# Kernel optimization log

Measured on AMD Instinct MI355X. Metric: run time of the kernel, lower is better.

## Reference

```python
import jax, jax.numpy as jnp
import numpy as np


def log_g(x):
    # log of g(x) = where(x>=0, x+0.5, sigmoid(x))
    return jnp.where(x >= 0, jnp.log(jnp.maximum(x, 0) + 0.5), -jax.nn.softplus(-x))


def setup_inputs() -> dict:
    key = jax.random.key(0)
    ks = jax.random.split(key, 6)
    B, S, D, H = 4, 4096, 1024, 1024
    x = jax.random.normal(ks[0], (B, S, D), dtype=jnp.float32)
    h0 = jax.random.normal(ks[1], (B, 1, H), dtype=jnp.float32)
    # Linear params (scaled like trained weights to keep activations tame)
    Wz = jax.random.normal(ks[2], (H, D), dtype=jnp.float32) * 0.02
    bz = jax.random.normal(ks[3], (H,), dtype=jnp.float32) * 0.02
    Wh = jax.random.normal(ks[4], (H, D), dtype=jnp.float32) * 0.02
    bh = jax.random.normal(ks[5], (H,), dtype=jnp.float32) * 0.02
    return {"x": x, "h0": h0, "Wz": Wz, "bz": bz, "Wh": Wh, "bh": bh}


def reference(x, h0, Wz, bz, Wh, bh):
    # x: [B,S,D], h0: [B,1,H]
    k = jnp.einsum('bsd,hd->bsh', x, Wz) + bz            # linear_z(x)
    log_z = -jax.nn.softplus(-k)                          # log sigmoid(k)
    log_coeffs = -jax.nn.softplus(k)                      # log (1 - sigmoid(k))
    log_h0 = log_g(h0)                                    # [B,1,H]
    log_tilde_h = log_g(jnp.einsum('bsd,hd->bsh', x, Wh) + bh)
    log_coeffs = jnp.pad(log_coeffs, ((0, 0), (1, 0), (0, 0)))  # prepend zero coeff
    log_values = jnp.concatenate([log_h0, log_z + log_tilde_h], axis=1)  # [B,S+1,H]
    # parallel scan in log space
    a_star = jnp.cumsum(log_coeffs, axis=1)
    log_h = a_star + jax.lax.cumlogsumexp(log_values - a_star, axis=1)
    h = jnp.exp(log_h)
    out = h[:, 1:]                                        # last seq_len steps
    return (out, out[:, -1:])
```

## Files before the change

kernel.cpp:

```cpp
#include <hip/hip_runtime.h>
#include <stdint.h>

typedef __attribute__((ext_vector_type(4))) float f32x4;
typedef __attribute__((ext_vector_type(8))) short bf16x8;
typedef __attribute__((ext_vector_type(4))) unsigned short u16x4;

constexpr int cB = 4, cS = 4096, cD = 1024, cH = 1024;
constexpr int cM = cB * cS;
constexpr int cK = cD;
constexpr int NCH = 64;
constexpr int CLEN = cS / NCH;

__device__ __forceinline__ unsigned short f2bf(float f) {
  union { float f; uint32_t u; } v; v.f = f;
  uint32_t r = v.u + 0x7FFFu + ((v.u >> 16) & 1u);
  return (unsigned short)(r >> 16);
}
__device__ __forceinline__ float bf2f(unsigned short h) {
  union { float f; uint32_t u; } v; v.u = ((uint32_t)h) << 16;
  return v.f;
}

__global__ void round_kernel(const float* __restrict__ src,
                             unsigned short* __restrict__ hi) {
  int i = (blockIdx.x * blockDim.x + threadIdx.x) * 4;
  f32x4 x = *(const f32x4*)(src + i);
  u16x4 h;
#pragma unroll
  for (int j = 0; j < 4; ++j) h[j] = f2bf(x[j]);
  *(u16x4*)(hi + i) = h;
}

constexpr int BM = 128, BN = 128, BK = 64;

__global__ __launch_bounds__(256, 2) void gemm_kernel(
    const unsigned short* __restrict__ xh,
    const unsigned short* __restrict__ wwh,
    const float* __restrict__ bz, const float* __restrict__ bhv,
    unsigned short* __restrict__ cbuf, unsigned short* __restrict__ gbuf,
    float* __restrict__ Pb, float* __restrict__ Qb)
{
  __shared__ unsigned short Ah[BM * BK], Bz[BN * BK], Bh[BN * BK];
  const int tid  = threadIdx.x;
  const int lane = tid & 63;
  const int wv   = tid >> 6;
  const int wr   = wv >> 1, wc = wv & 1;

  const int bid = blockIdx.x;
  const int xcd = bid & 7;
  const int idx = bid >> 3;
  const int mt  = xcd * 16 + (idx >> 3);
  const int nt  = idx & 7;
  const int m0 = mt * BM, n0 = nt * BN;
  const int fr = lane & 15, fq = lane >> 4;

  f32x4 accz[4][4] = {};
  f32x4 acch[4][4] = {};

  const int srow = tid >> 3;
  const int scol = (((tid & 7) ^ (srow & 7)) << 3);

  const unsigned short* gA = xh  + (size_t)m0 * cK;
  const unsigned short* gZ = wwh + (size_t)n0 * cK;
  const unsigned short* gH = wwh + (size_t)(cH + n0) * cK;

  for (int kt = 0; kt < cK / BK; ++kt) {
    const int k0 = kt * BK;
    __syncthreads();
#pragma unroll
    for (int r = 0; r < 4; ++r) {
      const int row = r * 32 + srow;
      const int ldsoff = r * 4096 + tid * 16;
      const size_t goff = (size_t)row * cK + k0 + scol;
      __builtin_amdgcn_global_load_lds((const __attribute__((address_space(1))) void*)(gA + goff),
        (__attribute__((address_space(3))) void*)((char*)Ah + ldsoff), 16, 0, 0);
      __builtin_amdgcn_global_load_lds((const __attribute__((address_space(1))) void*)(gZ + goff),
        (__attribute__((address_space(3))) void*)((char*)Bz + ldsoff), 16, 0, 0);
      __builtin_amdgcn_global_load_lds((const __attribute__((address_space(1))) void*)(gH + goff),
        (__attribute__((address_space(3))) void*)((char*)Bh + ldsoff), 16, 0, 0);
    }
    __syncthreads();
#pragma unroll
    for (int kk = 0; kk < BK / 32; ++kk) {
      bf16x8 fa[4], fz[4], fh[4];
#pragma unroll
      for (int i = 0; i < 4; ++i) {
        const int ar = wr * 64 + i * 16 + fr;
        const int ca = (kk * 64 + fq * 16) ^ ((ar & 7) << 4);
        fa[i] = *(const bf16x8*)((const char*)Ah + ar * 128 + ca);
        const int br = wc * 64 + i * 16 + fr;
        const int cb = (kk * 64 + fq * 16) ^ ((br & 7) << 4);
        fz[i] = *(const bf16x8*)((const char*)Bz + br * 128 + cb);
        fh[i] = *(const bf16x8*)((const char*)Bh + br * 128 + cb);
      }
#pragma unroll
      for (int i = 0; i < 4; ++i)
#pragma unroll
        for (int j = 0; j < 4; ++j) {
          accz[i][j] = __builtin_amdgcn_mfma_f32_16x16x32_bf16(fa[i], fz[j], accz[i][j], 0, 0, 0);
          acch[i][j] = __builtin_amdgcn_mfma_f32_16x16x32_bf16(fa[i], fh[j], acch[i][j], 0, 0, 0);
        }
    }
  }

  const int b  = mt >> 5;
  const int ch = (mt & 31) * 2 + wr;
#pragma unroll
  for (int j = 0; j < 4; ++j) {
    const int n = n0 + wc * 64 + j * 16 + fr;
    const float bz_n = bz[n];
    const float bh_n = bhv[n];
    float psg[4], qsg[4];
#pragma unroll
    for (int i = 0; i < 4; ++i) {
      float p = 1.0f, q = 0.0f;
#pragma unroll
      for (int rg = 0; rg < 4; ++rg) {
        const int m = m0 + wr * 64 + i * 16 + fq * 4 + rg;
        const float kv = accz[i][j][rg] + bz_n;
        const float av = acch[i][j][rg] + bh_n;
        const float c = 1.0f / (1.0f + expf(kv));
        const float g = (av >= 0.0f) ? (av + 0.5f) : (1.0f / (1.0f + expf(-av)));
        cbuf[(size_t)m * cH + n] = f2bf(c);
        gbuf[(size_t)m * cH + n] = f2bf(g);
        q = c * q + (1.0f - c) * g;
        p = c * p;
      }
      float pp = __shfl_xor(p, 16), qq = __shfl_xor(q, 16);
      if (fq & 1) { q = q + p * qq; } else { q = qq + pp * q; }
      p = p * pp;
      pp = __shfl_xor(p, 32); qq = __shfl_xor(q, 32);
      if (fq & 2) { q = q + p * qq; } else { q = qq + pp * q; }
      p = p * pp;
      psg[i] = p; qsg[i] = q;
    }
    float P = psg[0], Q = qsg[0];
#pragma unroll
    for (int i = 1; i < 4; ++i) { Q = qsg[i] + psg[i] * Q; P = psg[i] * P; }
    if (fq == 0) {
      const size_t o = ((size_t)b * NCH + ch) * cH + n;
      Pb[o] = P; Qb[o] = Q;
    }
  }
}

__global__ void scan_prefix_kernel(const float* __restrict__ h0,
                                   const float* __restrict__ Pb, const float* __restrict__ Qb,
                                   float* __restrict__ hin) {
  const int idx = blockIdx.x * blockDim.x + threadIdx.x;
  const int b = idx / cH, h = idx % cH;
  float x = h0[idx];
  float hc = (x >= 0.0f) ? (x + 0.5f) : (1.0f / (1.0f + expf(-x)));
#pragma unroll 4
  for (int j = 0; j < NCH; ++j) {
    size_t o = ((size_t)b * NCH + j) * cH + h;
    hin[o] = hc;
    hc = Qb[o] + Pb[o] * hc;
  }
}

__global__ void scan_write_kernel(const unsigned short* __restrict__ cb,
                                  const unsigned short* __restrict__ gb,
                                  const float* __restrict__ hin, float* __restrict__ out) {
  const int bc = blockIdx.x;
  const int b = bc / NCH, ch = bc % NCH;
  const int h4 = threadIdx.x * 4;
  f32x4 hc = *(const f32x4*)(hin + ((size_t)b * NCH + ch) * cH + h4);
  size_t base = ((size_t)b * cS + (size_t)ch * CLEN) * cH + h4;
#pragma unroll 4
  for (int i = 0; i < CLEN; ++i) {
    u16x4 cv = *(const u16x4*)(cb + base + (size_t)i * cH);
    u16x4 gv = *(const u16x4*)(gb + base + (size_t)i * cH);
#pragma unroll
    for (int j = 0; j < 4; ++j) {
      const float c = bf2f(cv[j]), g = bf2f(gv[j]);
      hc[j] = c * hc[j] + (1.0f - c) * g;
    }
    *(f32x4*)(out + base + (size_t)i * cH) = hc;
  }
  if (ch == NCH - 1) {
    *(f32x4*)(out + (size_t)cM * cH + (size_t)b * cH + h4) = hc;
  }
}

extern "C" void kernel_launch(void* const* d_in, const int* in_sizes, int n_in,
                              void* d_out, int out_size, void* d_ws, size_t ws_size,
                              hipStream_t stream) {
  const float* x   = (const float*)d_in[0];
  const float* h0  = (const float*)d_in[1];
  const float* Wz  = (const float*)d_in[2];
  const float* bz  = (const float*)d_in[3];
  const float* Wh  = (const float*)d_in[4];
  const float* bh  = (const float*)d_in[5];

  char* ws = (char*)d_ws;
  unsigned short* xh   = (unsigned short*)(ws);
  unsigned short* wwh  = (unsigned short*)(ws + (((size_t)32) << 20));
  unsigned short* cbuf = (unsigned short*)(ws + (((size_t)40) << 20));
  unsigned short* gbuf = (unsigned short*)(ws + (((size_t)72) << 20));
  float* Pb   = (float*)(ws + (((size_t)104) << 20));
  float* Qb   = (float*)(ws + (((size_t)105) << 20));
  float* hin  = (float*)(ws + (((size_t)106) << 20));
  float* out  = (float*)d_out;

  round_kernel<<<cM * cK / 1024, 256, 0, stream>>>(x, xh);
  round_kernel<<<cH * cK / 1024, 256, 0, stream>>>(Wz, wwh);
  round_kernel<<<cH * cK / 1024, 256, 0, stream>>>(Wh, wwh + (size_t)cH * cK);
  gemm_kernel<<<(cM / BM) * (cH / BN), 256, 0, stream>>>(xh, wwh, bz, bh, cbuf, gbuf, Pb, Qb);
  scan_prefix_kernel<<<cB * cH / 256, 256, 0, stream>>>(h0, Pb, Qb, hin);
  scan_write_kernel<<<cB * NCH, 256, 0, stream>>>(cbuf, gbuf, hin, out);
}
```

Before: 144.0 us.

## Interleave c/g into one packed buffer and parallelize chunk prefix scan with wave shuffles

The GEMM epilogue now writes bf16 c and g packed into a single 32-bit word per element, so there is one store stream instead of two, and scan_write does one 16-byte load per step. The chunk-level prefix scan becomes a wavefront-wide shuffle scan over the 64 chunks per (batch, hidden) column, replacing a 64-step serial loop per thread. The parallel scan uses strided loads across chunks and more waves, which trades serial latency for more scattered memory access.

```diff
diff --git a/kernel.cpp b/kernel.cpp
--- a/kernel.cpp
+++ b/kernel.cpp
@@ -4,6 +4,7 @@
 typedef __attribute__((ext_vector_type(4))) float f32x4;
 typedef __attribute__((ext_vector_type(8))) short bf16x8;
 typedef __attribute__((ext_vector_type(4))) unsigned short u16x4;
+typedef __attribute__((ext_vector_type(4))) unsigned int u32x4;
 
 constexpr int cB = 4, cS = 4096, cD = 1024, cH = 1024;
 constexpr int cM = cB * cS;
@@ -37,7 +38,7 @@
     const unsigned short* __restrict__ xh,
     const unsigned short* __restrict__ wwh,
     const float* __restrict__ bz, const float* __restrict__ bhv,
-    unsigned short* __restrict__ cbuf, unsigned short* __restrict__ gbuf,
+    unsigned int* __restrict__ cgbuf,
     float* __restrict__ Pb, float* __restrict__ Qb)
 {
   __shared__ unsigned short Ah[BM * BK], Bz[BN * BK], Bh[BN * BK];
@@ -121,8 +122,7 @@
         const float av = acch[i][j][rg] + bh_n;
         const float c = 1.0f / (1.0f + expf(kv));
         const float g = (av >= 0.0f) ? (av + 0.5f) : (1.0f / (1.0f + expf(-av)));
-        cbuf[(size_t)m * cH + n] = f2bf(c);
-        gbuf[(size_t)m * cH + n] = f2bf(g);
+        cgbuf[(size_t)m * cH + n] = ((uint32_t)f2bf(g) << 16) | (uint32_t)f2bf(c);
         q = c * q + (1.0f - c) * g;
         p = c * p;
       }
@@ -147,20 +147,24 @@
 __global__ void scan_prefix_kernel(const float* __restrict__ h0,
                                    const float* __restrict__ Pb, const float* __restrict__ Qb,
                                    float* __restrict__ hin) {
-  const int idx = blockIdx.x * blockDim.x + threadIdx.x;
-  const int b = idx / cH, h = idx % cH;
-  float x = h0[idx];
-  float hc = (x >= 0.0f) ? (x + 0.5f) : (1.0f / (1.0f + expf(-x)));
-#pragma unroll 4
-  for (int j = 0; j < NCH; ++j) {
-    size_t o = ((size_t)b * NCH + j) * cH + h;
-    hin[o] = hc;
-    hc = Qb[o] + Pb[o] * hc;
-  }
-}
-
-__global__ void scan_write_kernel(const unsigned short* __restrict__ cb,
-                                  const unsigned short* __restrict__ gb,
+  const int wid  = (blockIdx.x * blockDim.x + threadIdx.x) >> 6;
+  const int lane = threadIdx.x & 63;
+  const int b = wid >> 10, h = wid & 1023;
+  const size_t o = ((size_t)b * NCH + lane) * cH + h;
+  float P = Pb[o], Q = Qb[o];
+#pragma unroll
+  for (int off = 1; off < 64; off <<= 1) {
+    float Po = __shfl_up(P, off), Qo = __shfl_up(Q, off);
+    if (lane >= off) { Q = P * Qo + Q; P = P * Po; }
+  }
+  float Pe = __shfl_up(P, 1), Qe = __shfl_up(Q, 1);
+  if (lane == 0) { Pe = 1.0f; Qe = 0.0f; }
+  const float x = h0[b * cH + h];
+  const float h0g = (x >= 0.0f) ? (x + 0.5f) : (1.0f / (1.0f + expf(-x)));
+  hin[o] = Pe * h0g + Qe;
+}
+
+__global__ void scan_write_kernel(const unsigned int* __restrict__ cg,
                                   const float* __restrict__ hin, float* __restrict__ out) {
   const int bc = blockIdx.x;
   const int b = bc / NCH, ch = bc % NCH;
@@ -169,11 +173,11 @@
   size_t base = ((size_t)b * cS + (size_t)ch * CLEN) * cH + h4;
 #pragma unroll 4
   for (int i = 0; i < CLEN; ++i) {
-    u16x4 cv = *(const u16x4*)(cb + base + (size_t)i * cH);
-    u16x4 gv = *(const u16x4*)(gb + base + (size_t)i * cH);
+    u32x4 v = *(const u32x4*)(cg + base + (size_t)i * cH);
 #pragma unroll
     for (int j = 0; j < 4; ++j) {
-      const float c = bf2f(cv[j]), g = bf2f(gv[j]);
+      const float c = bf2f((unsigned short)(v[j] & 0xFFFFu));
+      const float g = bf2f((unsigned short)(v[j] >> 16));
       hc[j] = c * hc[j] + (1.0f - c) * g;
     }
     *(f32x4*)(out + base + (size_t)i * cH) = hc;
@@ -196,8 +200,7 @@
   char* ws = (char*)d_ws;
   unsigned short* xh   = (unsigned short*)(ws);
   unsigned short* wwh  = (unsigned short*)(ws + (((size_t)32) << 20));
-  unsigned short* cbuf = (unsigned short*)(ws + (((size_t)40) << 20));
-  unsigned short* gbuf = (unsigned short*)(ws + (((size_t)72) << 20));
+  unsigned int*   cgbuf= (unsigned int*)(ws + (((size_t)40) << 20));
   float* Pb   = (float*)(ws + (((size_t)104) << 20));
   float* Qb   = (float*)(ws + (((size_t)105) << 20));
   float* hin  = (float*)(ws + (((size_t)106) << 20));
@@ -206,7 +209,7 @@
   round_kernel<<<cM * cK / 1024, 256, 0, stream>>>(x, xh);
   round_kernel<<<cH * cK / 1024, 256, 0, stream>>>(Wz, wwh);
   round_kernel<<<cH * cK / 1024, 256, 0, stream>>>(Wh, wwh + (size_t)cH * cK);
-  gemm_kernel<<<(cM / BM) * (cH / BN), 256, 0, stream>>>(xh, wwh, bz, bh, cbuf, gbuf, Pb, Qb);
-  scan_prefix_kernel<<<cB * cH / 256, 256, 0, stream>>>(h0, Pb, Qb, hin);
-  scan_write_kernel<<<cB * NCH, 256, 0, stream>>>(cbuf, gbuf, hin, out);
-}
+  gemm_kernel<<<(cM / BM) * (cH / BN), 256, 0, stream>>>(xh, wwh, bz, bh, cgbuf, Pb, Qb);
+  scan_prefix_kernel<<<cB * cH * 64 / 256, 256, 0, stream>>>(h0, Pb, Qb, hin);
+  scan_write_kernel<<<cB * NCH, 256, 0, stream>>>(cgbuf, hin, out);
+}
```

Result: faster. 141.1 us (-2.0%).
